# Kernel optimization log

Hardware: AMD Instinct MI355X
Metric: run time of the kernel (lower is better)

The kernel has to match this reference:

```python
import jax, jax.numpy as jnp
import numpy as np

C_IN = 256
RED = 8
C_QK = C_IN // RED  # 32


def setup_inputs() -> dict:
    key = jax.random.key(0)
    ks = jax.random.split(key, 7)
    B, C, H, W = 4, C_IN, 64, 64
    s = 1.0 / np.sqrt(C)
    return {
        "x": jax.random.normal(ks[0], (B, C, H, W), dtype=jnp.float32),
        "wq": jax.random.uniform(ks[1], (C_QK, C), jnp.float32, -s, s),
        "bq": jax.random.uniform(ks[2], (C_QK,), jnp.float32, -s, s),
        "wk": jax.random.uniform(ks[3], (C_QK, C), jnp.float32, -s, s),
        "bk": jax.random.uniform(ks[4], (C_QK,), jnp.float32, -s, s),
        "wv": jax.random.uniform(ks[5], (C, C), jnp.float32, -s, s),
        "bv": jax.random.uniform(ks[6], (C,), jnp.float32, -s, s),
        "gamma": jnp.zeros((1,), dtype=jnp.float32),
    }


def reference(x, wq, bq, wk, bk, wv, bv, gamma):
    B, C, H, W = x.shape
    N = H * W
    xf = x.reshape(B, C, N)  # flatten spatial tokens
    # 1x1 convs == per-pixel linear projections over channels
    q = jnp.einsum("oc,bcn->bno", wq, xf) + bq            # (B, N, C_qk)
    k = jnp.einsum("oc,bcn->bon", wk, xf) + bk[:, None]   # (B, C_qk, N)
    v = jnp.einsum("oc,bcn->bon", wv, xf) + bv[:, None]   # (B, C, N)
    # unscaled attention: softmax over keys (last dim)
    attn = jax.nn.softmax(jnp.einsum("bio,boj->bij", q, k), axis=-1)  # (B, N, N)
    # attended[b,c,i] = sum_j v[b,c,j] * attn[b,i,j]  (bmm with attn^T)
    attended = jnp.einsum("bcj,bij->bci", v, attn).reshape(B, C, H, W)
    output = gamma[0] * attended + x
    attention_map = attn.mean(axis=1).reshape(B, H, W)
    return output, attention_map
```

## Files before the change

kernel.cpp:

```cpp
#include <hip/hip_runtime.h>


#define B_   4
#define C_   256
#define N_   4096
#define CQK_ 32
#define BCN_ (B_*C_*N_)
#define BN_  (B_*N_)
#define TP_  260
#define LOG2E 1.4426950408889634f

typedef __attribute__((ext_vector_type(8))) short short8v;
typedef __attribute__((ext_vector_type(4))) short short4v;
typedef __attribute__((ext_vector_type(4))) float f32x4;
typedef unsigned short ushort_t;

__device__ __forceinline__ ushort_t f2bf(float f) {
  unsigned u = __builtin_bit_cast(unsigned, f);
  u += 0x7FFFu + ((u >> 16) & 1u);
  return (ushort_t)(u >> 16);
}
__device__ __forceinline__ float bf2f(ushort_t h) {
  unsigned u = ((unsigned)h) << 16;
  return __builtin_bit_cast(float, u);
}
__device__ __forceinline__ short8v ld8f(const float* p) {
  float4 a = *(const float4*)p, b = *(const float4*)(p + 4);
  short8v r;
  r[0]=f2bf(a.x); r[1]=f2bf(a.y); r[2]=f2bf(a.z); r[3]=f2bf(a.w);
  r[4]=f2bf(b.x); r[5]=f2bf(b.y); r[6]=f2bf(b.z); r[7]=f2bf(b.w);
  return r;
}
__device__ __forceinline__ short8v ld8lds(const ushort_t* p) {
  short4v lo = *(const short4v*)p, hi = *(const short4v*)(p + 4);
  return __builtin_shufflevector(lo, hi, 0, 1, 2, 3, 4, 5, 6, 7);
}

__global__ __launch_bounds__(256) void
k_prep(const float* __restrict__ x,
       const float* __restrict__ wq, const float* __restrict__ bq,
       const float* __restrict__ wk, const float* __restrict__ bk,
       const float* __restrict__ wv, const float* __restrict__ bv,
       const float* __restrict__ gamma,
       float* __restrict__ out, float* __restrict__ l,
       ushort_t* __restrict__ qb, ushort_t* __restrict__ kb,
       float* __restrict__ v_t) {
  __shared__ ushort_t xs[32 * TP_];
  int blk = blockIdx.x, tid = threadIdx.x;
  int b = blk >> 7, n0 = (blk & 127) << 5;
#pragma unroll
  for (int it = 0; it < 8; ++it) {
    int flat = it * 256 + tid;
    int c = flat >> 3, t4 = flat & 7;
    size_t off = ((size_t)(b * C_) + c) * N_ + n0 + t4 * 4;
    float4 v = *(const float4*)(x + off);
    *(float4*)(out + off) = v;
    ushort_t* dst = &xs[(t4 * 4) * TP_ + c];
    dst[0]        = f2bf(v.x);
    dst[TP_]      = f2bf(v.y);
    dst[2 * TP_]  = f2bf(v.z);
    dst[3 * TP_]  = f2bf(v.w);
  }
  if (blk < 64) {
    int idx = blk * 256 + tid;
    l[idx] = 0.0f;
    out[BCN_ + idx] = 0.0f;
  }
  __syncthreads();

  int wave = tid >> 6, lane = tid & 63;
  int col16 = lane & 15, quad = lane >> 4;
  int g = wave & 1;
  bool isq = wave < 2;
  int tok_l = g * 16 + col16;
  int n = n0 + tok_l;
  short8v bfr[8];
#pragma unroll
  for (int ks = 0; ks < 8; ++ks)
    bfr[ks] = ld8lds(&xs[tok_l * TP_ + ks * 32 + quad * 8]);

  const float* wrow = isq ? wq : wk;
  const float* bias = isq ? bq : bk;
  ushort_t* dst = isq ? qb : kb;
#pragma unroll
  for (int mt = 0; mt < 2; ++mt) {
    f32x4 c = {0.f, 0.f, 0.f, 0.f};
#pragma unroll
    for (int ks = 0; ks < 8; ++ks) {
      short8v afr = ld8f(wrow + (mt * 16 + col16) * C_ + ks * 32 + quad * 8);
      c = __builtin_amdgcn_mfma_f32_16x16x32_bf16(afr, bfr[ks], c, 0, 0, 0);
    }
    int co = mt * 16 + quad * 4;
    ushort4 pk;
    if (isq) {
      pk.x = f2bf((c[0] + bias[co + 0]) * LOG2E);
      pk.y = f2bf((c[1] + bias[co + 1]) * LOG2E);
      pk.z = f2bf((c[2] + bias[co + 2]) * LOG2E);
      pk.w = f2bf((c[3] + bias[co + 3]) * LOG2E);
    } else {
      pk.x = f2bf(c[0] + bias[co + 0]); pk.y = f2bf(c[1] + bias[co + 1]);
      pk.z = f2bf(c[2] + bias[co + 2]); pk.w = f2bf(c[3] + bias[co + 3]);
    }
    *(ushort4*)(dst + ((size_t)(b * N_) + n) * CQK_ + co) = pk;
  }

  if (gamma[0] != 0.0f) {
    int half = wave >> 1;
    for (int vt = 0; vt < 8; ++vt) {
      int tile = half * 8 + vt;
      f32x4 c = {0.f, 0.f, 0.f, 0.f};
#pragma unroll
      for (int ks = 0; ks < 8; ++ks) {
        short8v afr = ld8f(wv + (tile * 16 + col16) * C_ + ks * 32 + quad * 8);
        c = __builtin_amdgcn_mfma_f32_16x16x32_bf16(afr, bfr[ks], c, 0, 0, 0);
      }
      int co = tile * 16 + quad * 4;
      float4 o;
      o.x = c[0] + bv[co];     o.y = c[1] + bv[co + 1];
      o.z = c[2] + bv[co + 2]; o.w = c[3] + bv[co + 3];
      *(float4*)(v_t + ((size_t)(b * N_) + n) * C_ + co) = o;
    }
  }
}

__global__ __launch_bounds__(256) void
k_rowsA(const ushort_t* __restrict__ qb, const ushort_t* __restrict__ kb,
        float* __restrict__ l) {
  int blk = blockIdx.x;
  int b = blk >> 8, rg = (blk >> 2) & 63, js = blk & 3;
  int wave = threadIdx.x >> 6, lane = threadIdx.x & 63;
  int col16 = lane & 15, quad = lane >> 4;
  const ushort_t* qbb = qb + (size_t)b * N_ * CQK_;
  const ushort_t* kbb = kb + (size_t)b * N_ * CQK_;
  int i_base = rg * 64;
  short8v a[4];
#pragma unroll
  for (int t = 0; t < 4; ++t)
    a[t] = *(const short8v*)(qbb + (i_base + t * 16 + col16) * CQK_ + quad * 8);
  float racc[16];
#pragma unroll
  for (int r = 0; r < 16; ++r) racc[r] = 0.0f;
  int j_base = js * 1024 + wave * 256;
#pragma unroll 4
  for (int t = 0; t < 16; ++t) {
    short8v bfr = *(const short8v*)(kbb + (j_base + t * 16 + col16) * CQK_ + quad * 8);
#pragma unroll
    for (int m = 0; m < 4; ++m) {
      f32x4 c = {0.f, 0.f, 0.f, 0.f};
      c = __builtin_amdgcn_mfma_f32_16x16x32_bf16(a[m], bfr, c, 0, 0, 0);
      racc[m * 4 + 0] += __builtin_amdgcn_exp2f(c[0]);
      racc[m * 4 + 1] += __builtin_amdgcn_exp2f(c[1]);
      racc[m * 4 + 2] += __builtin_amdgcn_exp2f(c[2]);
      racc[m * 4 + 3] += __builtin_amdgcn_exp2f(c[3]);
    }
  }
#pragma unroll
  for (int r = 0; r < 16; ++r) {
    float v = racc[r];
    v += __shfl_xor(v, 1); v += __shfl_xor(v, 2);
    v += __shfl_xor(v, 4); v += __shfl_xor(v, 8);
    racc[r] = v;
  }
  if (col16 == 0) {
    float* lb = l + b * N_ + i_base;
#pragma unroll
    for (int m = 0; m < 4; ++m)
#pragma unroll
      for (int rr = 0; rr < 4; ++rr)
        atomicAdd(&lb[m * 16 + quad * 4 + rr], racc[m * 4 + rr]);
  }
}

__global__ __launch_bounds__(256) void
k_mapB(const ushort_t* __restrict__ qb, const ushort_t* __restrict__ kb,
       const float* __restrict__ l, float* __restrict__ map) {
  int blk = blockIdx.x;
  int b = blk >> 8, jg = (blk >> 4) & 15, isp = blk & 15;
  int wave = threadIdx.x >> 6, lane = threadIdx.x & 63;
  int col16 = lane & 15, quad = lane >> 4;
  const ushort_t* qbb = qb + (size_t)b * N_ * CQK_;
  const ushort_t* kbb = kb + (size_t)b * N_ * CQK_;
  int j_base = jg * 256 + wave * 64;
  short8v a[4];
#pragma unroll
  for (int t = 0; t < 4; ++t)
    a[t] = *(const short8v*)(kbb + (j_base + t * 16 + col16) * CQK_ + quad * 8);
  float csum[16];
#pragma unroll
  for (int r = 0; r < 16; ++r) csum[r] = 0.0f;
  int i_base = isp * 256;
#pragma unroll 4
  for (int t = 0; t < 16; ++t) {
    int i0 = i_base + t * 16;
    short8v bfr = *(const short8v*)(qbb + (i0 + col16) * CQK_ + quad * 8);
    float llog = -__builtin_amdgcn_logf(l[b * N_ + i0 + col16]);
    f32x4 cinit = {llog, llog, llog, llog};
#pragma unroll
    for (int m = 0; m < 4; ++m) {
      f32x4 c = __builtin_amdgcn_mfma_f32_16x16x32_bf16(a[m], bfr, cinit, 0, 0, 0);
      csum[m * 4 + 0] += __builtin_amdgcn_exp2f(c[0]);
      csum[m * 4 + 1] += __builtin_amdgcn_exp2f(c[1]);
      csum[m * 4 + 2] += __builtin_amdgcn_exp2f(c[2]);
      csum[m * 4 + 3] += __builtin_amdgcn_exp2f(c[3]);
    }
  }
#pragma unroll
  for (int r = 0; r < 16; ++r) {
    float v = csum[r];
    v += __shfl_xor(v, 1); v += __shfl_xor(v, 2);
    v += __shfl_xor(v, 4); v += __shfl_xor(v, 8);
    csum[r] = v;
  }
  if (col16 == 0) {
    float* mp = map + b * N_ + j_base;
#pragma unroll
    for (int m = 0; m < 4; ++m)
#pragma unroll
      for (int rr = 0; rr < 4; ++rr)
        atomicAdd(&mp[m * 16 + quad * 4 + rr], csum[m * 4 + rr] * (1.0f / (float)N_));
  }
}

__global__ __launch_bounds__(256) void
k_pv(const ushort_t* __restrict__ qb, const ushort_t* __restrict__ kb,
     const float* __restrict__ v_t, const float* __restrict__ l,
     const float* __restrict__ gamma, float* __restrict__ out) {
  if (gamma[0] == 0.0f) return;
  __shared__ float qs[32 * CQK_];
  __shared__ float invl[32];
  __shared__ float ps[32 * 256];
  int blk = blockIdx.x;
  int b = blk >> 9, i0 = ((blk >> 2) & 127) << 5, jsp = blk & 3;
  int tid = threadIdx.x;
  for (int r = tid; r < 32 * CQK_; r += 256)
    qs[r] = bf2f(qb[((size_t)(b * N_) + i0) * CQK_ + r]);
  if (tid < 32) invl[tid] = 1.0f / l[b * N_ + i0 + tid];
  __syncthreads();
  float g = gamma[0];
  float acc[32];
#pragma unroll
  for (int i = 0; i < 32; ++i) acc[i] = 0.0f;
  for (int jt = jsp * 4; jt < jsp * 4 + 4; ++jt) {
    int j = jt * 256 + tid;
    const ushort_t* krow = kb + ((size_t)(b * N_) + j) * CQK_;
    float kcol[CQK_];
#pragma unroll
    for (int o = 0; o < CQK_; ++o) kcol[o] = bf2f(krow[o]);
#pragma unroll
    for (int i = 0; i < 32; ++i) {
      float s = 0.0f;
#pragma unroll
      for (int o = 0; o < CQK_; ++o) s += qs[i * CQK_ + o] * kcol[o];
      ps[i * 256 + tid] = __builtin_amdgcn_exp2f(s) * invl[i];
    }
    __syncthreads();
    const float* vtb = v_t + ((size_t)(b * N_) + jt * 256) * C_;
    for (int jj = 0; jj < 256; ++jj) {
      float vv = vtb[(size_t)jj * C_ + tid];
#pragma unroll
      for (int i = 0; i < 32; ++i) acc[i] += ps[i * 256 + jj] * vv;
    }
    __syncthreads();
  }
  float* ob = out + ((size_t)(b * C_) + tid) * N_ + i0;
#pragma unroll
  for (int i = 0; i < 32; ++i) atomicAdd(&ob[i], g * acc[i]);
}

extern "C" void kernel_launch(void* const* d_in, const int* in_sizes, int n_in,
                              void* d_out, int out_size, void* d_ws, size_t ws_size,
                              hipStream_t stream) {
  const float* x     = (const float*)d_in[0];
  const float* wq    = (const float*)d_in[1];
  const float* bq    = (const float*)d_in[2];
  const float* wk    = (const float*)d_in[3];
  const float* bk    = (const float*)d_in[4];
  const float* wv    = (const float*)d_in[5];
  const float* bv    = (const float*)d_in[6];
  const float* gamma = (const float*)d_in[7];
  float* out = (float*)d_out;
  float* wsf = (float*)d_ws;
  float*    l   = wsf;
  ushort_t* qb  = (ushort_t*)(wsf + 16384);
  ushort_t* kb  = (ushort_t*)(wsf + 16384 + 262144);
  float*    v_t = wsf + 16384 + 2 * 262144;

  k_prep <<< 512, 256, 0, stream>>>(x, wq, bq, wk, bk, wv, bv, gamma,
                                    out, l, qb, kb, v_t);
  k_rowsA<<<1024, 256, 0, stream>>>(qb, kb, l);
  k_mapB <<<1024, 256, 0, stream>>>(qb, kb, l, out + BCN_);
  k_pv   <<<2048, 256, 0, stream>>>(qb, kb, v_t, l, gamma, out);
}
```

Measured before the change: 122.9 us.

## Replace global atomics with in-block LDS reductions and precompute log row sums

Row-sum and column-map kernels now give each 512-thread block a full key/query range, so each block reduces its 8 waves' partial sums through shared memory and writes results directly. This removes the global atomicAdds and the zero-initialisation pass in the prep kernel. The row kernel also stores -log(l) once, so the map kernel no longer computes a log on every tile iteration. Prep is split into smaller 16-token blocks for more parallelism, at the cost of fewer blocks (512) for the two attention-stat kernels and longer serial loops per wave.

```diff
diff --git a/kernel.cpp b/kernel.cpp
--- a/kernel.cpp
+++ b/kernel.cpp
@@ -42,16 +42,16 @@
        const float* __restrict__ wk, const float* __restrict__ bk,
        const float* __restrict__ wv, const float* __restrict__ bv,
        const float* __restrict__ gamma,
-       float* __restrict__ out, float* __restrict__ l,
+       float* __restrict__ out,
        ushort_t* __restrict__ qb, ushort_t* __restrict__ kb,
        float* __restrict__ v_t) {
-  __shared__ ushort_t xs[32 * TP_];
+  __shared__ ushort_t xs[16 * TP_];
   int blk = blockIdx.x, tid = threadIdx.x;
-  int b = blk >> 7, n0 = (blk & 127) << 5;
-#pragma unroll
-  for (int it = 0; it < 8; ++it) {
+  int b = blk >> 8, n0 = (blk & 255) << 4;
+#pragma unroll
+  for (int it = 0; it < 4; ++it) {
     int flat = it * 256 + tid;
-    int c = flat >> 3, t4 = flat & 7;
+    int c = flat >> 2, t4 = flat & 3;
     size_t off = ((size_t)(b * C_) + c) * N_ + n0 + t4 * 4;
     float4 v = *(const float4*)(x + off);
     *(float4*)(out + off) = v;
@@ -61,163 +61,168 @@
     dst[2 * TP_]  = f2bf(v.z);
     dst[3 * TP_]  = f2bf(v.w);
   }
-  if (blk < 64) {
-    int idx = blk * 256 + tid;
-    l[idx] = 0.0f;
-    out[BCN_ + idx] = 0.0f;
-  }
   __syncthreads();
 
   int wave = tid >> 6, lane = tid & 63;
   int col16 = lane & 15, quad = lane >> 4;
-  int g = wave & 1;
   bool isq = wave < 2;
-  int tok_l = g * 16 + col16;
-  int n = n0 + tok_l;
+  int mt = wave & 1;
   short8v bfr[8];
 #pragma unroll
   for (int ks = 0; ks < 8; ++ks)
-    bfr[ks] = ld8lds(&xs[tok_l * TP_ + ks * 32 + quad * 8]);
+    bfr[ks] = ld8lds(&xs[col16 * TP_ + ks * 32 + quad * 8]);
 
   const float* wrow = isq ? wq : wk;
   const float* bias = isq ? bq : bk;
   ushort_t* dst = isq ? qb : kb;
-#pragma unroll
-  for (int mt = 0; mt < 2; ++mt) {
-    f32x4 c = {0.f, 0.f, 0.f, 0.f};
-#pragma unroll
-    for (int ks = 0; ks < 8; ++ks) {
-      short8v afr = ld8f(wrow + (mt * 16 + col16) * C_ + ks * 32 + quad * 8);
-      c = __builtin_amdgcn_mfma_f32_16x16x32_bf16(afr, bfr[ks], c, 0, 0, 0);
-    }
-    int co = mt * 16 + quad * 4;
-    ushort4 pk;
-    if (isq) {
-      pk.x = f2bf((c[0] + bias[co + 0]) * LOG2E);
-      pk.y = f2bf((c[1] + bias[co + 1]) * LOG2E);
-      pk.z = f2bf((c[2] + bias[co + 2]) * LOG2E);
-      pk.w = f2bf((c[3] + bias[co + 3]) * LOG2E);
-    } else {
-      pk.x = f2bf(c[0] + bias[co + 0]); pk.y = f2bf(c[1] + bias[co + 1]);
-      pk.z = f2bf(c[2] + bias[co + 2]); pk.w = f2bf(c[3] + bias[co + 3]);
-    }
-    *(ushort4*)(dst + ((size_t)(b * N_) + n) * CQK_ + co) = pk;
-  }
+  f32x4 c = {0.f, 0.f, 0.f, 0.f};
+#pragma unroll
+  for (int ks = 0; ks < 8; ++ks) {
+    short8v afr = ld8f(wrow + (mt * 16 + col16) * C_ + ks * 32 + quad * 8);
+    c = __builtin_amdgcn_mfma_f32_16x16x32_bf16(afr, bfr[ks], c, 0, 0, 0);
+  }
+  int co = mt * 16 + quad * 4;
+  ushort4 pk;
+  if (isq) {
+    pk.x = f2bf((c[0] + bias[co + 0]) * LOG2E);
+    pk.y = f2bf((c[1] + bias[co + 1]) * LOG2E);
+    pk.z = f2bf((c[2] + bias[co + 2]) * LOG2E);
+    pk.w = f2bf((c[3] + bias[co + 3]) * LOG2E);
+  } else {
+    pk.x = f2bf(c[0] + bias[co + 0]); pk.y = f2bf(c[1] + bias[co + 1]);
+    pk.z = f2bf(c[2] + bias[co + 2]); pk.w = f2bf(c[3] + bias[co + 3]);
+  }
+  *(ushort4*)(dst + ((size_t)(b * N_) + n0 + col16) * CQK_ + co) = pk;
 
   if (gamma[0] != 0.0f) {
-    int half = wave >> 1;
-    for (int vt = 0; vt < 8; ++vt) {
-      int tile = half * 8 + vt;
-      f32x4 c = {0.f, 0.f, 0.f, 0.f};
+#pragma unroll
+    for (int vt = 0; vt < 4; ++vt) {
+      int tile = wave * 4 + vt;
+      f32x4 cv = {0.f, 0.f, 0.f, 0.f};
 #pragma unroll
       for (int ks = 0; ks < 8; ++ks) {
         short8v afr = ld8f(wv + (tile * 16 + col16) * C_ + ks * 32 + quad * 8);
-        c = __builtin_amdgcn_mfma_f32_16x16x32_bf16(afr, bfr[ks], c, 0, 0, 0);
+        cv = __builtin_amdgcn_mfma_f32_16x16x32_bf16(afr, bfr[ks], cv, 0, 0, 0);
       }
-      int co = tile * 16 + quad * 4;
+      int cvo = tile * 16 + quad * 4;
       float4 o;
-      o.x = c[0] + bv[co];     o.y = c[1] + bv[co + 1];
-      o.z = c[2] + bv[co + 2]; o.w = c[3] + bv[co + 3];
-      *(float4*)(v_t + ((size_t)(b * N_) + n) * C_ + co) = o;
+      o.x = cv[0] + bv[cvo];     o.y = cv[1] + bv[cvo + 1];
+      o.z = cv[2] + bv[cvo + 2]; o.w = cv[3] + bv[cvo + 3];
+      *(float4*)(v_t + ((size_t)(b * N_) + n0 + col16) * C_ + cvo) = o;
     }
   }
 }
 
-__global__ __launch_bounds__(256) void
+__global__ __launch_bounds__(512) void
 k_rowsA(const ushort_t* __restrict__ qb, const ushort_t* __restrict__ kb,
-        float* __restrict__ l) {
+        float* __restrict__ l, float* __restrict__ llog) {
+  __shared__ float red[8][32];
   int blk = blockIdx.x;
-  int b = blk >> 8, rg = (blk >> 2) & 63, js = blk & 3;
-  int wave = threadIdx.x >> 6, lane = threadIdx.x & 63;
+  int b = blk >> 7, rg = blk & 127;
+  int tid = threadIdx.x, wave = tid >> 6, lane = tid & 63;
   int col16 = lane & 15, quad = lane >> 4;
   const ushort_t* qbb = qb + (size_t)b * N_ * CQK_;
   const ushort_t* kbb = kb + (size_t)b * N_ * CQK_;
-  int i_base = rg * 64;
-  short8v a[4];
-#pragma unroll
-  for (int t = 0; t < 4; ++t)
-    a[t] = *(const short8v*)(qbb + (i_base + t * 16 + col16) * CQK_ + quad * 8);
-  float racc[16];
-#pragma unroll
-  for (int r = 0; r < 16; ++r) racc[r] = 0.0f;
-  int j_base = js * 1024 + wave * 256;
+  int i_base = rg * 32;
+  short8v a0 = *(const short8v*)(qbb + (size_t)(i_base + col16) * CQK_ + quad * 8);
+  short8v a1 = *(const short8v*)(qbb + (size_t)(i_base + 16 + col16) * CQK_ + quad * 8);
+  float racc[8];
+#pragma unroll
+  for (int r = 0; r < 8; ++r) racc[r] = 0.0f;
+  const f32x4 z = {0.f, 0.f, 0.f, 0.f};
+  const ushort_t* kp = kbb + (size_t)(wave * 512 + col16) * CQK_ + quad * 8;
 #pragma unroll 4
-  for (int t = 0; t < 16; ++t) {
-    short8v bfr = *(const short8v*)(kbb + (j_base + t * 16 + col16) * CQK_ + quad * 8);
-#pragma unroll
-    for (int m = 0; m < 4; ++m) {
-      f32x4 c = {0.f, 0.f, 0.f, 0.f};
-      c = __builtin_amdgcn_mfma_f32_16x16x32_bf16(a[m], bfr, c, 0, 0, 0);
-      racc[m * 4 + 0] += __builtin_amdgcn_exp2f(c[0]);
-      racc[m * 4 + 1] += __builtin_amdgcn_exp2f(c[1]);
-      racc[m * 4 + 2] += __builtin_amdgcn_exp2f(c[2]);
-      racc[m * 4 + 3] += __builtin_amdgcn_exp2f(c[3]);
-    }
-  }
-#pragma unroll
-  for (int r = 0; r < 16; ++r) {
+  for (int t = 0; t < 32; ++t) {
+    short8v bfr = *(const short8v*)(kp + (size_t)t * 16 * CQK_);
+    f32x4 c0 = __builtin_amdgcn_mfma_f32_16x16x32_bf16(a0, bfr, z, 0, 0, 0);
+    f32x4 c1 = __builtin_amdgcn_mfma_f32_16x16x32_bf16(a1, bfr, z, 0, 0, 0);
+    racc[0] += __builtin_amdgcn_exp2f(c0[0]);
+    racc[1] += __builtin_amdgcn_exp2f(c0[1]);
+    racc[2] += __builtin_amdgcn_exp2f(c0[2]);
+    racc[3] += __builtin_amdgcn_exp2f(c0[3]);
+    racc[4] += __builtin_amdgcn_exp2f(c1[0]);
+    racc[5] += __builtin_amdgcn_exp2f(c1[1]);
+    racc[6] += __builtin_amdgcn_exp2f(c1[2]);
+    racc[7] += __builtin_amdgcn_exp2f(c1[3]);
+  }
+#pragma unroll
+  for (int r = 0; r < 8; ++r) {
     float v = racc[r];
     v += __shfl_xor(v, 1); v += __shfl_xor(v, 2);
     v += __shfl_xor(v, 4); v += __shfl_xor(v, 8);
     racc[r] = v;
   }
   if (col16 == 0) {
-    float* lb = l + b * N_ + i_base;
-#pragma unroll
-    for (int m = 0; m < 4; ++m)
+#pragma unroll
+    for (int m = 0; m < 2; ++m)
 #pragma unroll
       for (int rr = 0; rr < 4; ++rr)
-        atomicAdd(&lb[m * 16 + quad * 4 + rr], racc[m * 4 + rr]);
-  }
-}
-
-__global__ __launch_bounds__(256) void
+        red[wave][m * 16 + quad * 4 + rr] = racc[m * 4 + rr];
+  }
+  __syncthreads();
+  if (tid < 32) {
+    float s = 0.0f;
+#pragma unroll
+    for (int w = 0; w < 8; ++w) s += red[w][tid];
+    l[b * N_ + i_base + tid] = s;
+    llog[b * N_ + i_base + tid] = -__builtin_amdgcn_logf(s);
+  }
+}
+
+__global__ __launch_bounds__(512) void
 k_mapB(const ushort_t* __restrict__ qb, const ushort_t* __restrict__ kb,
-       const float* __restrict__ l, float* __restrict__ map) {
+       const float* __restrict__ llog, float* __restrict__ map) {
+  __shared__ float red[8][32];
   int blk = blockIdx.x;
-  int b = blk >> 8, jg = (blk >> 4) & 15, isp = blk & 15;
-  int wave = threadIdx.x >> 6, lane = threadIdx.x & 63;
+  int b = blk >> 7, jg = blk & 127;
+  int tid = threadIdx.x, wave = tid >> 6, lane = tid & 63;
   int col16 = lane & 15, quad = lane >> 4;
   const ushort_t* qbb = qb + (size_t)b * N_ * CQK_;
   const ushort_t* kbb = kb + (size_t)b * N_ * CQK_;
-  int j_base = jg * 256 + wave * 64;
-  short8v a[4];
-#pragma unroll
-  for (int t = 0; t < 4; ++t)
-    a[t] = *(const short8v*)(kbb + (j_base + t * 16 + col16) * CQK_ + quad * 8);
-  float csum[16];
-#pragma unroll
-  for (int r = 0; r < 16; ++r) csum[r] = 0.0f;
-  int i_base = isp * 256;
+  int j_base = jg * 32;
+  short8v a0 = *(const short8v*)(kbb + (size_t)(j_base + col16) * CQK_ + quad * 8);
+  short8v a1 = *(const short8v*)(kbb + (size_t)(j_base + 16 + col16) * CQK_ + quad * 8);
+  float csum[8];
+#pragma unroll
+  for (int r = 0; r < 8; ++r) csum[r] = 0.0f;
+  const float* lp = llog + b * N_ + wave * 512 + col16;
+  const ushort_t* qp = qbb + (size_t)(wave * 512 + col16) * CQK_ + quad * 8;
 #pragma unroll 4
-  for (int t = 0; t < 16; ++t) {
-    int i0 = i_base + t * 16;
-    short8v bfr = *(const short8v*)(qbb + (i0 + col16) * CQK_ + quad * 8);
-    float llog = -__builtin_amdgcn_logf(l[b * N_ + i0 + col16]);
-    f32x4 cinit = {llog, llog, llog, llog};
-#pragma unroll
-    for (int m = 0; m < 4; ++m) {
-      f32x4 c = __builtin_amdgcn_mfma_f32_16x16x32_bf16(a[m], bfr, cinit, 0, 0, 0);
-      csum[m * 4 + 0] += __builtin_amdgcn_exp2f(c[0]);
-      csum[m * 4 + 1] += __builtin_amdgcn_exp2f(c[1]);
-      csum[m * 4 + 2] += __builtin_amdgcn_exp2f(c[2]);
-      csum[m * 4 + 3] += __builtin_amdgcn_exp2f(c[3]);
-    }
-  }
-#pragma unroll
-  for (int r = 0; r < 16; ++r) {
+  for (int t = 0; t < 32; ++t) {
+    short8v bfr = *(const short8v*)(qp + (size_t)t * 16 * CQK_);
+    float ll = lp[t * 16];
+    f32x4 ci = {ll, ll, ll, ll};
+    f32x4 c0 = __builtin_amdgcn_mfma_f32_16x16x32_bf16(a0, bfr, ci, 0, 0, 0);
+    f32x4 c1 = __builtin_amdgcn_mfma_f32_16x16x32_bf16(a1, bfr, ci, 0, 0, 0);
+    csum[0] += __builtin_amdgcn_exp2f(c0[0]);
+    csum[1] += __builtin_amdgcn_exp2f(c0[1]);
+    csum[2] += __builtin_amdgcn_exp2f(c0[2]);
+    csum[3] += __builtin_amdgcn_exp2f(c0[3]);
+    csum[4] += __builtin_amdgcn_exp2f(c1[0]);
+    csum[5] += __builtin_amdgcn_exp2f(c1[1]);
+    csum[6] += __builtin_amdgcn_exp2f(c1[2]);
+    csum[7] += __builtin_amdgcn_exp2f(c1[3]);
+  }
+#pragma unroll
+  for (int r = 0; r < 8; ++r) {
     float v = csum[r];
     v += __shfl_xor(v, 1); v += __shfl_xor(v, 2);
     v += __shfl_xor(v, 4); v += __shfl_xor(v, 8);
     csum[r] = v;
   }
   if (col16 == 0) {
-    float* mp = map + b * N_ + j_base;
-#pragma unroll
-    for (int m = 0; m < 4; ++m)
+#pragma unroll
+    for (int m = 0; m < 2; ++m)
 #pragma unroll
       for (int rr = 0; rr < 4; ++rr)
-        atomicAdd(&mp[m * 16 + quad * 4 + rr], csum[m * 4 + rr] * (1.0f / (float)N_));
+        red[wave][m * 16 + quad * 4 + rr] = csum[m * 4 + rr];
+  }
+  __syncthreads();
+  if (tid < 32) {
+    float s = 0.0f;
+#pragma unroll
+    for (int w = 0; w < 8; ++w) s += red[w][tid];
+    map[b * N_ + j_base + tid] = s * (1.0f / (float)N_);
   }
 }
 
@@ -280,14 +285,15 @@
   const float* gamma = (const float*)d_in[7];
   float* out = (float*)d_out;
   float* wsf = (float*)d_ws;
-  float*    l   = wsf;
-  ushort_t* qb  = (ushort_t*)(wsf + 16384);
-  ushort_t* kb  = (ushort_t*)(wsf + 16384 + 262144);
-  float*    v_t = wsf + 16384 + 2 * 262144;
-
-  k_prep <<< 512, 256, 0, stream>>>(x, wq, bq, wk, bk, wv, bv, gamma,
-                                    out, l, qb, kb, v_t);
-  k_rowsA<<<1024, 256, 0, stream>>>(qb, kb, l);
-  k_mapB <<<1024, 256, 0, stream>>>(qb, kb, l, out + BCN_);
+  float*    l    = wsf;
+  float*    llog = wsf + 16384;
+  ushort_t* qb   = (ushort_t*)(wsf + 32768);
+  ushort_t* kb   = (ushort_t*)(wsf + 32768 + 262144);
+  float*    v_t  = wsf + 32768 + 2 * 262144;
+
+  k_prep <<<1024, 256, 0, stream>>>(x, wq, bq, wk, bk, wv, bv, gamma,
+                                    out, qb, kb, v_t);
+  k_rowsA<<< 512, 512, 0, stream>>>(qb, kb, l, llog);
+  k_mapB <<< 512, 512, 0, stream>>>(qb, kb, llog, out + BCN_);
   k_pv   <<<2048, 256, 0, stream>>>(qb, kb, v_t, l, gamma, out);
 }
```

Result: faster. 113.0 us (median of 2 runs) (-8.1%).
